# Performance work log

Measured on AMD Instinct MI355X. Metric: run time of the kernel, lower is better.

The kernel has to match this reference:

```python
import jax, jax.numpy as jnp
import numpy as np


def _cdist(a, b):
    # Euclidean pairwise distances, [N, M]
    d2 = (jnp.sum(a * a, axis=1)[:, None]
          + jnp.sum(b * b, axis=1)[None, :]
          - 2.0 * (a @ b.T))
    return jnp.sqrt(jnp.maximum(d2, 0.0))


def setup_inputs() -> dict:
    key = jax.random.key(0)
    k1, k2 = jax.random.split(key)
    N, M, D = 12288, 12288, 3
    true_pos = jax.random.normal(k1, (N, D), dtype=jnp.float32)
    pred_pos = jax.random.normal(k2, (M, D), dtype=jnp.float32)
    return {"true_pos": true_pos, "pred_pos": pred_pos}


def reference(true_pos, pred_pos):
    dists = _cdist(true_pos.astype(jnp.float32), pred_pos.astype(jnp.float32))
    mins = jnp.min(dists, axis=1)        # per true point -> nearest pred
    mins_seeds = jnp.min(dists, axis=0)  # per pred point -> nearest true
    loss = jnp.mean(mins)
    loss_seeds = jnp.mean(mins_seeds)
    just_in_case_losses = (loss, loss_seeds)
    # use_loss=True branch
    return (loss + loss_seeds, mins_seeds, just_in_case_losses)
```

## Files before the change

kernel.cpp:

```cpp
#include <hip/hip_runtime.h>
#include <cfloat>

typedef __bf16 bf16x8 __attribute__((ext_vector_type(8)));
typedef unsigned short ushort8 __attribute__((ext_vector_type(8)));
typedef float f32x16 __attribute__((ext_vector_type(16)));

#define S_SLICES 4

static __device__ __forceinline__ unsigned short f2bf(float x) {
    unsigned u = __float_as_uint(x);
    return (unsigned short)((u + 0x7FFFu + ((u >> 16) & 1u)) >> 16);
}
static __device__ __forceinline__ float bfbits2f(unsigned short h) {
    return __uint_as_float(((unsigned)h) << 16);
}

__global__ __launch_bounds__(256) void prep_kernel(
    const float* __restrict__ A, const float* __restrict__ B,
    ushort8* __restrict__ RFA, ushort8* __restrict__ CFA,
    ushort8* __restrict__ RFB, ushort8* __restrict__ CFB,
    float* __restrict__ hdr, int n, int m, int RTn, int RTm)
{
    const int i = blockIdx.x * 256 + threadIdx.x;
    if (i < 8) hdr[i] = 0.f;
    const unsigned short one = 0x3F80;

#pragma unroll
    for (int side = 0; side < 2; ++side) {
        const int cntPts = side ? RTm * 32 : RTn * 32;
        if (i >= cntPts) continue;
        const float* P = side ? B : A;
        const int lim = side ? m : n;
        ushort8* RF = side ? RFB : RFA;
        ushort8* CF = side ? CFB : CFA;

        float x = 0.f, y = 0.f, z = 0.f, nrm = 1e30f;
        if (i < lim) { x = P[3*i]; y = P[3*i+1]; z = P[3*i+2];
                       nrm = fmaf(x, x, fmaf(y, y, z * z)); }
        const unsigned short hx = f2bf(x), hy = f2bf(y), hz = f2bf(z);
        const unsigned short lx = f2bf(x - bfbits2f(hx)),
                             ly = f2bf(y - bfbits2f(hy)),
                             lz = f2bf(z - bfbits2f(hz));
        const unsigned short nhx = f2bf(-2.f * bfbits2f(hx)),
                             nhy = f2bf(-2.f * bfbits2f(hy)),
                             nhz = f2bf(-2.f * bfbits2f(hz));
        const unsigned short nlx = f2bf(-2.f * bfbits2f(lx)),
                             nly = f2bf(-2.f * bfbits2f(ly)),
                             nlz = f2bf(-2.f * bfbits2f(lz));
        float r = nrm;
        const unsigned short s1 = f2bf(r); r -= bfbits2f(s1);
        const unsigned short s2 = f2bf(r); r -= bfbits2f(s2);
        const unsigned short s3 = f2bf(r);

        const int t = i >> 5, l5 = i & 31;
        ushort8 rq0 = { nhx, nhy, nhz, nhx, nhy, nhz, nlx, nly };
        ushort8 rq1 = { nlz, s1, s2, s3, one, one, one, 0 };
        RF[t * 64 + l5]      = rq0;
        RF[t * 64 + 32 + l5] = rq1;
        ushort8 cq0 = { hx, hy, hz, lx, ly, lz, hx, hy };
        ushort8 cq1 = { hz, one, one, one, s1, s2, s3, 0 };
        CF[t * 64 + l5]      = cq0;
        CF[t * 64 + 32 + l5] = cq1;
    }
}

#define MINC(C)                                             \
    _Pragma("unroll")                                       \
    for (int r = 0; r < 16; ++r) macc[r] = fminf(macc[r], (C)[r]);

__global__ __launch_bounds__(256, 4) void pairmin_kernel(
    const bf16x8* __restrict__ RFA, const bf16x8* __restrict__ CFA,
    const bf16x8* __restrict__ RFB, const bf16x8* __restrict__ CFB,
    float* __restrict__ sbuf, int RTn, int RTm)
{
    const int lane = threadIdx.x & 63;
    const int wave = threadIdx.x >> 6;

    const bf16x8* RF; const bf16x8* CF; float* sb; int rtCount, ctCount, stride;
    if (blockIdx.z == 0) { RF = RFA; CF = CFB; rtCount = RTn; ctCount = RTm;
                           sb = sbuf; stride = RTn * 32; }
    else                 { RF = RFB; CF = CFA; rtCount = RTm; ctCount = RTn;
                           sb = sbuf + (size_t)S_SLICES * RTn * 32;
                           stride = RTm * 32; }

    const int rt = blockIdx.x * 4 + wave;
    if (rt >= rtCount) return;
    sb += (size_t)blockIdx.y * stride;

    const int ctPer = (ctCount + S_SLICES - 1) / S_SLICES;
    const int ctBeg = min(blockIdx.y * ctPer, ctCount);
    const int ctEnd = min(ctBeg + ctPer, ctCount);

    const bf16x8 afrag = RF[rt * 64 + lane];
    const f32x16 zc = {};

    float macc[16];
#pragma unroll
    for (int r = 0; r < 16; ++r) macc[r] = FLT_MAX;

    if (ctBeg < ctEnd) {
        int ct = ctBeg;
        const int last = ctEnd - 1;
        bf16x8 q0 = CF[(size_t)ct * 64 + lane];
        bf16x8 q1 = CF[(size_t)min(ct + 1, last) * 64 + lane];
        bf16x8 q2 = CF[(size_t)min(ct + 2, last) * 64 + lane];
        bf16x8 q3 = CF[(size_t)min(ct + 3, last) * 64 + lane];
        f32x16 C0 = __builtin_amdgcn_mfma_f32_32x32x16_bf16(afrag, q0, zc, 0, 0, 0);
        f32x16 C1 = __builtin_amdgcn_mfma_f32_32x32x16_bf16(afrag, q1, zc, 0, 0, 0);

        for (; ct + 7 < ctEnd; ct += 4) {
            q0 = CF[(size_t)(ct + 4) * 64 + lane];
            MINC(C0);
            C0 = __builtin_amdgcn_mfma_f32_32x32x16_bf16(afrag, q2, zc, 0, 0, 0);
            q1 = CF[(size_t)(ct + 5) * 64 + lane];
            MINC(C1);
            C1 = __builtin_amdgcn_mfma_f32_32x32x16_bf16(afrag, q3, zc, 0, 0, 0);
            q2 = CF[(size_t)(ct + 6) * 64 + lane];
            MINC(C0);
            C0 = __builtin_amdgcn_mfma_f32_32x32x16_bf16(afrag, q0, zc, 0, 0, 0);
            q3 = CF[(size_t)(ct + 7) * 64 + lane];
            MINC(C1);
            C1 = __builtin_amdgcn_mfma_f32_32x32x16_bf16(afrag, q1, zc, 0, 0, 0);
        }
        MINC(C0);
        MINC(C1);
        if (ct + 2 < ctEnd) {
            const f32x16 C =
                __builtin_amdgcn_mfma_f32_32x32x16_bf16(afrag, q2, zc, 0, 0, 0);
            MINC(C);
        }
        if (ct + 3 < ctEnd) {
            const f32x16 C =
                __builtin_amdgcn_mfma_f32_32x32x16_bf16(afrag, q3, zc, 0, 0, 0);
            MINC(C);
        }
        for (int t = ct + 4; t < ctEnd; ++t) {
            const bf16x8 b = CF[(size_t)t * 64 + lane];
            const f32x16 C =
                __builtin_amdgcn_mfma_f32_32x32x16_bf16(afrag, b, zc, 0, 0, 0);
            MINC(C);
        }
    }

#pragma unroll
    for (int r = 0; r < 16; ++r) {
        float v = macc[r];
        v = fminf(v, __shfl_xor(v, 1, 64));
        v = fminf(v, __shfl_xor(v, 2, 64));
        v = fminf(v, __shfl_xor(v, 4, 64));
        v = fminf(v, __shfl_xor(v, 8, 64));
        v = fminf(v, __shfl_xor(v, 16, 64));
        macc[r] = v;
    }
    if ((lane & 31) == 0) {
        const int q4 = (lane >> 5) * 4;
        float* dst = sb + rt * 32;
#pragma unroll
        for (int r = 0; r < 16; ++r)
            dst[(r & 3) + 8 * (r >> 2) + q4] = macc[r];
    }
}

__global__ __launch_bounds__(256) void finalize_kernel(
    const float* __restrict__ sbuf, float* __restrict__ hdr,
    float* __restrict__ out, int n, int m, int RTn, int RTm)
{
    const int i = blockIdx.x * 256 + threadIdx.x;
    const int strideA = RTn * 32, strideB = RTm * 32;
    const float* sbB = sbuf + (size_t)S_SLICES * strideA;

    float sa = 0.f, sb_ = 0.f;
    if (i < n) {
        float s = FLT_MAX;
#pragma unroll
        for (int k = 0; k < S_SLICES; ++k) s = fminf(s, sbuf[(size_t)k * strideA + i]);
        sa = sqrtf(fmaxf(s, 0.f));
    }
    if (i < m) {
        float s = FLT_MAX;
#pragma unroll
        for (int k = 0; k < S_SLICES; ++k) s = fminf(s, sbB[(size_t)k * strideB + i]);
        const float v = sqrtf(fmaxf(s, 0.f));
        out[1 + i] = v;
        sb_ = v;
    }

#pragma unroll
    for (int off = 32; off > 0; off >>= 1) {
        sa  += __shfl_down(sa,  off, 64);
        sb_ += __shfl_down(sb_, off, 64);
    }
    __shared__ float reda[4], redb[4];
    const int wave = threadIdx.x >> 6;
    const int lane = threadIdx.x & 63;
    if (lane == 0) { reda[wave] = sa; redb[wave] = sb_; }
    __syncthreads();

    if (threadIdx.x == 0) {
        const float ta = reda[0] + reda[1] + reda[2] + reda[3];
        const float tb = redb[0] + redb[1] + redb[2] + redb[3];
        atomicAdd(&hdr[0], ta);
        atomicAdd(&hdr[1], tb);
        __threadfence();
        const unsigned ticket = atomicAdd((unsigned*)&hdr[2], 1u);
        if (ticket == (unsigned)(gridDim.x - 1)) {
            const float fa = atomicAdd(&hdr[0], 0.f);
            const float fb = atomicAdd(&hdr[1], 0.f);
            const float loss = fa / (float)n;
            const float loss_seeds = fb / (float)m;
            out[0] = loss + loss_seeds;
            out[1 + m] = loss;
            out[2 + m] = loss_seeds;
        }
    }
}

extern "C" void kernel_launch(void* const* d_in, const int* in_sizes, int n_in,
                              void* d_out, int out_size, void* d_ws, size_t ws_size,
                              hipStream_t stream) {
    const int n = in_sizes[0] / 3;
    const int m = in_sizes[1] / 3;
    const float* A = (const float*)d_in[0];
    const float* B = (const float*)d_in[1];
    float* out = (float*)d_out;

    const int RTn = (n + 31) / 32, RTm = (m + 31) / 32;
    char* p = (char*)d_ws;
    float*   hdr  = (float*)p;    p += 64;
    float*   sbuf = (float*)p;    p += (size_t)S_SLICES * (RTn + RTm) * 32 * 4;
    ushort8* RFA  = (ushort8*)p;  p += (size_t)RTn * 64 * 16;
    ushort8* CFA  = (ushort8*)p;  p += (size_t)RTn * 64 * 16;
    ushort8* RFB  = (ushort8*)p;  p += (size_t)RTm * 64 * 16;
    ushort8* CFB  = (ushort8*)p;

    const int maxPts = ((RTn > RTm) ? RTn : RTm) * 32;
    prep_kernel<<<(maxPts + 255) / 256, 256, 0, stream>>>(
        A, B, RFA, CFA, RFB, CFB, hdr, n, m, RTn, RTm);

    const int maxRT = (RTn > RTm) ? RTn : RTm;
    dim3 grid((maxRT + 3) / 4, S_SLICES, 2);
    pairmin_kernel<<<grid, 256, 0, stream>>>(
        (const bf16x8*)RFA, (const bf16x8*)CFA,
        (const bf16x8*)RFB, (const bf16x8*)CFB, sbuf, RTn, RTm);

    const int maxnm = (n > m) ? n : m;
    finalize_kernel<<<(maxnm + 255) / 256, 256, 0, stream>>>(
        sbuf, hdr, out, n, m, RTn, RTm);
}
```

Before: 77.23 us.

## Process two row tiles per wave to reuse column fragment loads

Each wave now handles a pair of 32-row tiles, so every loaded column fragment feeds two MFMAs instead of one. This halves global/L2 traffic per MFMA. To keep the grid size up, the column range is split into 8 slices instead of 4, and the occupancy hint drops from 4 to 3 blocks per CU. The cost is more accumulator registers per wave and twice as many partial-min slices for finalize to reduce.

```diff
diff --git a/kernel.cpp b/kernel.cpp
--- a/kernel.cpp
+++ b/kernel.cpp
@@ -5,7 +5,7 @@
 typedef unsigned short ushort8 __attribute__((ext_vector_type(8)));
 typedef float f32x16 __attribute__((ext_vector_type(16)));
 
-#define S_SLICES 4
+#define S_SLICES 8
 
 static __device__ __forceinline__ unsigned short f2bf(float x) {
     unsigned u = __float_as_uint(x);
@@ -64,11 +64,15 @@
     }
 }
 
-#define MINC(C)                                             \
+#define MFMA(a, b) __builtin_amdgcn_mfma_f32_32x32x16_bf16((a), (b), zc, 0, 0, 0)
+#define MIN0(C)                                             \
     _Pragma("unroll")                                       \
-    for (int r = 0; r < 16; ++r) macc[r] = fminf(macc[r], (C)[r]);
-
-__global__ __launch_bounds__(256, 4) void pairmin_kernel(
+    for (int r = 0; r < 16; ++r) macc0[r] = fminf(macc0[r], (C)[r]);
+#define MIN1(C)                                             \
+    _Pragma("unroll")                                       \
+    for (int r = 0; r < 16; ++r) macc1[r] = fminf(macc1[r], (C)[r]);
+
+__global__ __launch_bounds__(256, 3) void pairmin_kernel(
     const bf16x8* __restrict__ RFA, const bf16x8* __restrict__ CFA,
     const bf16x8* __restrict__ RFB, const bf16x8* __restrict__ CFB,
     float* __restrict__ sbuf, int RTn, int RTm)
@@ -83,20 +87,24 @@
                            sb = sbuf + (size_t)S_SLICES * RTn * 32;
                            stride = RTm * 32; }
 
-    const int rt = blockIdx.x * 4 + wave;
-    if (rt >= rtCount) return;
+    const int RTP = (rtCount + 1) >> 1;
+    const int rtPair = blockIdx.x * 4 + wave;
+    if (rtPair >= RTP) return;
+    const int rt0 = rtPair * 2;
+    const int rt1 = min(rt0 + 1, rtCount - 1);
     sb += (size_t)blockIdx.y * stride;
 
     const int ctPer = (ctCount + S_SLICES - 1) / S_SLICES;
     const int ctBeg = min(blockIdx.y * ctPer, ctCount);
     const int ctEnd = min(ctBeg + ctPer, ctCount);
 
-    const bf16x8 afrag = RF[rt * 64 + lane];
+    const bf16x8 a0 = RF[rt0 * 64 + lane];
+    const bf16x8 a1 = RF[rt1 * 64 + lane];
     const f32x16 zc = {};
 
-    float macc[16];
-#pragma unroll
-    for (int r = 0; r < 16; ++r) macc[r] = FLT_MAX;
+    float macc0[16], macc1[16];
+#pragma unroll
+    for (int r = 0; r < 16; ++r) { macc0[r] = FLT_MAX; macc1[r] = FLT_MAX; }
 
     if (ctBeg < ctEnd) {
         int ct = ctBeg;
@@ -105,59 +113,60 @@
         bf16x8 q1 = CF[(size_t)min(ct + 1, last) * 64 + lane];
         bf16x8 q2 = CF[(size_t)min(ct + 2, last) * 64 + lane];
         bf16x8 q3 = CF[(size_t)min(ct + 3, last) * 64 + lane];
-        f32x16 C0 = __builtin_amdgcn_mfma_f32_32x32x16_bf16(afrag, q0, zc, 0, 0, 0);
-        f32x16 C1 = __builtin_amdgcn_mfma_f32_32x32x16_bf16(afrag, q1, zc, 0, 0, 0);
+        f32x16 C0a = MFMA(a0, q0), C0b = MFMA(a1, q0);
+        f32x16 C1a = MFMA(a0, q1), C1b = MFMA(a1, q1);
 
         for (; ct + 7 < ctEnd; ct += 4) {
             q0 = CF[(size_t)(ct + 4) * 64 + lane];
-            MINC(C0);
-            C0 = __builtin_amdgcn_mfma_f32_32x32x16_bf16(afrag, q2, zc, 0, 0, 0);
+            MIN0(C0a); MIN1(C0b);
+            C0a = MFMA(a0, q2); C0b = MFMA(a1, q2);
             q1 = CF[(size_t)(ct + 5) * 64 + lane];
-            MINC(C1);
-            C1 = __builtin_amdgcn_mfma_f32_32x32x16_bf16(afrag, q3, zc, 0, 0, 0);
+            MIN0(C1a); MIN1(C1b);
+            C1a = MFMA(a0, q3); C1b = MFMA(a1, q3);
             q2 = CF[(size_t)(ct + 6) * 64 + lane];
-            MINC(C0);
-            C0 = __builtin_amdgcn_mfma_f32_32x32x16_bf16(afrag, q0, zc, 0, 0, 0);
+            MIN0(C0a); MIN1(C0b);
+            C0a = MFMA(a0, q0); C0b = MFMA(a1, q0);
             q3 = CF[(size_t)(ct + 7) * 64 + lane];
-            MINC(C1);
-            C1 = __builtin_amdgcn_mfma_f32_32x32x16_bf16(afrag, q1, zc, 0, 0, 0);
-        }
-        MINC(C0);
-        MINC(C1);
+            MIN0(C1a); MIN1(C1b);
+            C1a = MFMA(a0, q1); C1b = MFMA(a1, q1);
+        }
+        MIN0(C0a); MIN1(C0b);
+        MIN0(C1a); MIN1(C1b);
         if (ct + 2 < ctEnd) {
-            const f32x16 C =
-                __builtin_amdgcn_mfma_f32_32x32x16_bf16(afrag, q2, zc, 0, 0, 0);
-            MINC(C);
+            C0a = MFMA(a0, q2); C0b = MFMA(a1, q2);
+            MIN0(C0a); MIN1(C0b);
         }
         if (ct + 3 < ctEnd) {
-            const f32x16 C =
-                __builtin_amdgcn_mfma_f32_32x32x16_bf16(afrag, q3, zc, 0, 0, 0);
-            MINC(C);
+            C0a = MFMA(a0, q3); C0b = MFMA(a1, q3);
+            MIN0(C0a); MIN1(C0b);
         }
         for (int t = ct + 4; t < ctEnd; ++t) {
             const bf16x8 b = CF[(size_t)t * 64 + lane];
-            const f32x16 C =
-                __builtin_amdgcn_mfma_f32_32x32x16_bf16(afrag, b, zc, 0, 0, 0);
-            MINC(C);
+            C0a = MFMA(a0, b); C0b = MFMA(a1, b);
+            MIN0(C0a); MIN1(C0b);
         }
     }
 
 #pragma unroll
     for (int r = 0; r < 16; ++r) {
-        float v = macc[r];
-        v = fminf(v, __shfl_xor(v, 1, 64));
-        v = fminf(v, __shfl_xor(v, 2, 64));
-        v = fminf(v, __shfl_xor(v, 4, 64));
-        v = fminf(v, __shfl_xor(v, 8, 64));
-        v = fminf(v, __shfl_xor(v, 16, 64));
-        macc[r] = v;
+        float v = macc0[r], w = macc1[r];
+        v = fminf(v, __shfl_xor(v, 1, 64));  w = fminf(w, __shfl_xor(w, 1, 64));
+        v = fminf(v, __shfl_xor(v, 2, 64));  w = fminf(w, __shfl_xor(w, 2, 64));
+        v = fminf(v, __shfl_xor(v, 4, 64));  w = fminf(w, __shfl_xor(w, 4, 64));
+        v = fminf(v, __shfl_xor(v, 8, 64));  w = fminf(w, __shfl_xor(w, 8, 64));
+        v = fminf(v, __shfl_xor(v, 16, 64)); w = fminf(w, __shfl_xor(w, 16, 64));
+        macc0[r] = v; macc1[r] = w;
     }
     if ((lane & 31) == 0) {
         const int q4 = (lane >> 5) * 4;
-        float* dst = sb + rt * 32;
-#pragma unroll
-        for (int r = 0; r < 16; ++r)
-            dst[(r & 3) + 8 * (r >> 2) + q4] = macc[r];
+        float* dst0 = sb + rt0 * 32;
+        float* dst1 = sb + rt1 * 32;
+#pragma unroll
+        for (int r = 0; r < 16; ++r) {
+            const int row = (r & 3) + 8 * (r >> 2) + q4;
+            dst0[row] = macc0[r];
+            dst1[row] = macc1[r];
+        }
     }
 }
 
@@ -238,7 +247,8 @@
         A, B, RFA, CFA, RFB, CFB, hdr, n, m, RTn, RTm);
 
     const int maxRT = (RTn > RTm) ? RTn : RTm;
-    dim3 grid((maxRT + 3) / 4, S_SLICES, 2);
+    const int maxRTP = (maxRT + 1) / 2;
+    dim3 grid((maxRTP + 3) / 4, S_SLICES, 2);
     pairmin_kernel<<<grid, 256, 0, stream>>>(
         (const bf16x8*)RFA, (const bf16x8*)CFA,
         (const bf16x8*)RFB, (const bf16x8*)CFB, sbuf, RTn, RTm);
```

After: 79.67 us. 1.03x slower.
